# Kernel optimization log

Hardware: AMD Instinct MI355X
Metric: run time of the kernel (lower is better)

Reference implementation:

```python
import jax, jax.numpy as jnp
import numpy as np

BS, IC, L = 8, 64, 32768
OC, K = 64, 3
STRIDE, PAD, DIL = 1, 1, 1
ALPHA = 0.5  # SmoothQuant scaling_factor
QMAX = 127.0  # symmetric int8 fake quant


def fake_quant(t):
    # per-tensor symmetric int8 fake quantization with straight-through estimator
    amax = jnp.max(jnp.abs(jax.lax.stop_gradient(t)))
    s = jnp.where(amax == 0, 1.0, amax / QMAX)
    q = jnp.clip(jnp.round(t / s), -QMAX, QMAX) * s
    return t + jax.lax.stop_gradient(q - t)


def setup_inputs() -> dict:
    key = jax.random.key(0)
    k1, k2, k3 = jax.random.split(key, 3)
    x = jax.random.normal(k1, (BS, IC, L), dtype=jnp.float32)
    weight = jax.random.normal(k2, (OC, IC, K), dtype=jnp.float32) * 0.05
    bias = jax.random.normal(k3, (OC,), dtype=jnp.float32) * 0.01
    return {"x": x, "weight": weight, "bias": bias}


def reference(x, weight, bias):
    bs, ic, length = x.shape
    out_len = (length + 2 * PAD - DIL * (K - 1) - 1) // STRIDE + 1
    # im2col / unfold: (bs, ic, K, out_len) with F.unfold's channel-major, kernel-pos-minor order
    xp = jnp.pad(x, ((0, 0), (0, 0), (PAD, PAD)))
    patches = jnp.stack(
        [xp[:, :, j * DIL : j * DIL + STRIDE * (out_len - 1) + 1 : STRIDE] for j in range(K)],
        axis=2,
    )  # (bs, ic, K, out_len)
    cols = patches.reshape(bs, ic * K, out_len).transpose(0, 2, 1).reshape(bs * out_len, ic * K)
    w = weight.reshape(OC, ic * K)
    # dynamic SmoothQuant scales (detached in original)
    w_scale = jnp.max(jnp.abs(jax.lax.stop_gradient(w)), axis=0)        # (ic*K,)
    act_scale = jnp.max(jnp.abs(jax.lax.stop_gradient(cols)), axis=0)   # (ic*K,)
    scale = act_scale ** ALPHA / w_scale ** (1.0 - ALPHA)
    scale = jnp.where(scale == 0, 1.0, scale)
    xq = fake_quant(cols / scale)
    wq = fake_quant(w * scale)
    out = xq @ wq.T  # (bs*out_len, OC)
    out = out.reshape(bs, out_len, OC).transpose(0, 2, 1) + bias[None, :, None]
    return out
```

## Files before the change

### kernel.cpp

```cpp
#include <hip/hip_runtime.h>

#define L_LEN 32768
#define QMAXF 127.0f
#define TPB 4

typedef __attribute__((ext_vector_type(4))) int v4i;


__global__ __launch_bounds__(1024) void actamax_kernel(const float* __restrict__ x,
                                                       float* __restrict__ wsf) {
    const int ic = blockIdx.x, b = blockIdx.y;
    const float4* row = (const float4*)(x + ((size_t)(b*64 + ic) << 15));
    float mA = 0.0f, mNF = 0.0f, mNL = 0.0f;
    #pragma unroll
    for (int i = 0; i < 8; ++i) {
        int f = threadIdx.x + (i << 10);
        float4 v = row[f];
        float ax = fabsf(v.x), ay = fabsf(v.y), az = fabsf(v.z), aw = fabsf(v.w);
        float m4 = fmaxf(fmaxf(ax, ay), fmaxf(az, aw));
        mA = fmaxf(mA, m4);
        if (f == 0) {
            mNF = fmaxf(mNF, fmaxf(ay, fmaxf(az, aw)));
            mNL = fmaxf(mNL, m4);
        } else if (f == 8191) {
            mNF = fmaxf(mNF, m4);
            mNL = fmaxf(mNL, fmaxf(ax, fmaxf(ay, az)));
        } else {
            mNF = fmaxf(mNF, m4);
            mNL = fmaxf(mNL, m4);
        }
    }
    #pragma unroll
    for (int off = 32; off; off >>= 1) {
        mA  = fmaxf(mA,  __shfl_down(mA,  off));
        mNF = fmaxf(mNF, __shfl_down(mNF, off));
        mNL = fmaxf(mNL, __shfl_down(mNL, off));
    }
    __shared__ float red[3][16];
    int wid = threadIdx.x >> 6;
    if ((threadIdx.x & 63) == 0) { red[0][wid] = mA; red[1][wid] = mNF; red[2][wid] = mNL; }
    __syncthreads();
    if (threadIdx.x == 0) {
        mA = red[0][0]; mNF = red[1][0]; mNL = red[2][0];
        #pragma unroll
        for (int i = 1; i < 16; ++i) {
            mA  = fmaxf(mA,  red[0][i]);
            mNF = fmaxf(mNF, red[1][i]);
            mNL = fmaxf(mNL, red[2][i]);
        }
        float* p = wsf + (ic*8 + b)*3;
        p[0] = mNL; p[1] = mA; p[2] = mNF;
    }
}

__global__ __launch_bounds__(256) void prep_kernel(const float* __restrict__ w,
                                                   float* __restrict__ wsf,
                                                   unsigned int* __restrict__ wsa) {
    __shared__ float scl[192];
    __shared__ float red[256];
    const int tid = threadIdx.x;
    float ax = 0.0f, aw = 0.0f;
    if (tid < 192) {
        float wsc = 0.0f;
        #pragma unroll 8
        for (int o = 0; o < 64; ++o) wsc = fmaxf(wsc, fabsf(w[o*192 + tid]));
        int ic = tid / 3, k = tid - ic*3;
        float asc = 0.0f;
        #pragma unroll
        for (int b = 0; b < 8; ++b) asc = fmaxf(asc, wsf[(ic*8 + b)*3 + k]);
        float sc = sqrtf(asc) / sqrtf(wsc);
        if (sc == 0.0f) sc = 1.0f;
        scl[tid] = sc;
        ax = asc / sc;
        aw = wsc * sc;
    }
    red[tid] = ax; __syncthreads();
    for (int s = 128; s; s >>= 1) { if (tid < s) red[tid] = fmaxf(red[tid], red[tid+s]); __syncthreads(); }
    float axm = red[0]; __syncthreads();
    red[tid] = aw; __syncthreads();
    for (int s = 128; s; s >>= 1) { if (tid < s) red[tid] = fmaxf(red[tid], red[tid+s]); __syncthreads(); }
    float awm = red[0];
    float s_x = (axm == 0.0f) ? 1.0f : axm / QMAXF;
    float s_w = (awm == 0.0f) ? 1.0f : awm / QMAXF;
    if (tid < 192) wsf[1536 + tid] = 1.0f / (scl[tid] * s_x);
    if (tid == 0)  wsf[1728] = s_x * s_w;
    __syncthreads();
    for (int idx = tid; idx < 3072; idx += 256) {
        int oc = idx / 48, dwi = idx - oc*48, j0 = dwi*4;
        unsigned pk = 0;
        #pragma unroll
        for (int bb = 0; bb < 4; ++bb) {
            int j = j0 + bb;
            float q = rintf((w[oc*192 + j] * scl[j]) / s_w);
            q = fminf(fmaxf(q, -QMAXF), QMAXF);
            pk |= (((unsigned)(int)q) & 255u) << (8*bb);
        }
        int mt = oc >> 4, m = oc & 15, c = j0 >> 4, s = c >> 2, kq = c & 3;
        wsa[((mt*3 + s)*64 + kq*16 + m)*4 + ((j0 & 15) >> 2)] = pk;
    }
}

__global__ __launch_bounds__(256) void conv_mfma_kernel(const float* __restrict__ x,
                                                        const float* __restrict__ bias,
                                                        const float* __restrict__ wsf,
                                                        const v4i* __restrict__ wsa,
                                                        float* __restrict__ out) {
    __shared__ int bsm[3072];
    const int tid  = threadIdx.x;
    const int b    = blockIdx.y;
    const int lane = tid & 63;
    const int wv   = tid >> 6;

    const int tq  = tid & 15;
    const int icg = tid >> 4;
    const int tb  = tq << 2;

    float xv[4][6];
    {
        const int t0 = (blockIdx.x * TPB) << 6;
        #pragma unroll
        for (int ici = 0; ici < 4; ++ici) {
            const float* rowp = x + (((size_t)(b*64 + icg*4 + ici)) << 15) + t0 + tb;
            float4 mid = *(const float4*)rowp;
            float lm = (t0 + tb > 0)           ? rowp[-1] : 0.0f;
            float rp = (t0 + tb + 4 < L_LEN)   ? rowp[4]  : 0.0f;
            xv[ici][0] = lm;    xv[ici][1] = mid.x; xv[ici][2] = mid.y;
            xv[ici][3] = mid.z; xv[ici][4] = mid.w; xv[ici][5] = rp;
        }
    }

    v4i afrag[12];
    #pragma unroll
    for (int i = 0; i < 12; ++i) afrag[i] = wsa[i*64 + lane];

    float rv[12];
    #pragma unroll
    for (int jj = 0; jj < 12; ++jj) rv[jj] = wsf[1536 + icg*12 + jj];
    const float sxw = wsf[1728];

    for (int it = 0; it < TPB; ++it) {
        const int t0c = (blockIdx.x * TPB + it) << 6;

        unsigned pkq[12];
        #pragma unroll
        for (int dt = 0; dt < 4; ++dt) {
            #pragma unroll
            for (int dw = 0; dw < 3; ++dw) {
                unsigned pk = 0;
                #pragma unroll
                for (int bb = 0; bb < 4; ++bb) {
                    int jloc = dw*4 + bb;
                    int ici = jloc / 3, k = jloc - ici*3;
                    float q = rintf(xv[ici][dt + k] * rv[jloc]);
                    q = fminf(fmaxf(q, -QMAXF), QMAXF);
                    pk |= (((unsigned)(int)q) & 255u) << (8*bb);
                }
                pkq[dt*3 + dw] = pk;
            }
        }

        if (it) __syncthreads();
        #pragma unroll
        for (int dt = 0; dt < 4; ++dt) {
            int t = tb + dt, wt = t >> 4, n = t & 15;
            #pragma unroll
            for (int dw = 0; dw < 3; ++dw) {
                int j0 = icg*12 + dw*4;
                int c = j0 >> 4, s = c >> 2, kq = c & 3;
                int G = (wt*3 + s)*64 + kq*16 + n;
                G ^= (G >> 6) & 7;
                bsm[G*4 + ((j0 & 15) >> 2)] = (int)pkq[dt*3 + dw];
            }
        }
        __syncthreads();

        if (it + 1 < TPB) {
            const int t0n = (blockIdx.x * TPB + it + 1) << 6;
            #pragma unroll
            for (int ici = 0; ici < 4; ++ici) {
                const float* rowp = x + (((size_t)(b*64 + icg*4 + ici)) << 15) + t0n + tb;
                float4 mid = *(const float4*)rowp;
                float lm = (t0n + tb > 0)          ? rowp[-1] : 0.0f;
                float rp = (t0n + tb + 4 < L_LEN)  ? rowp[4]  : 0.0f;
                xv[ici][0] = lm;    xv[ici][1] = mid.x; xv[ici][2] = mid.y;
                xv[ici][3] = mid.z; xv[ici][4] = mid.w; xv[ici][5] = rp;
            }
        }

        v4i acc[4];
        #pragma unroll
        for (int mt = 0; mt < 4; ++mt) acc[mt] = (v4i){0,0,0,0};
        const v4i* bsmv = (const v4i*)bsm;
        #pragma unroll
        for (int s = 0; s < 3; ++s) {
            int Gr = (wv*3 + s)*64 + lane;
            Gr ^= (wv*3 + s) & 7;
            v4i bf = bsmv[Gr];
            #pragma unroll
            for (int mt = 0; mt < 4; ++mt)
                acc[mt] = __builtin_amdgcn_mfma_i32_16x16x64_i8(afrag[mt*3 + s], bf, acc[mt], 0, 0, 0);
        }

        const int tg   = t0c + (wv << 4) + (lane & 15);
        const int rowq = (lane >> 4) << 2;
        #pragma unroll
        for (int mt = 0; mt < 4; ++mt) {
            #pragma unroll
            for (int i = 0; i < 4; ++i) {
                int oc = mt*16 + rowq + i;
                out[(((size_t)(b*64 + oc)) << 15) + tg] = (float)acc[mt][i] * sxw + bias[oc];
            }
        }
    }
}

extern "C" void kernel_launch(void* const* d_in, const int* in_sizes, int n_in,
                              void* d_out, int out_size, void* d_ws, size_t ws_size,
                              hipStream_t stream) {
    const float* x    = (const float*)d_in[0];
    const float* w    = (const float*)d_in[1];
    const float* bias = (const float*)d_in[2];
    float* out = (float*)d_out;
    float* wsf = (float*)d_ws;
    unsigned int* wsa = (unsigned int*)((char*)d_ws + 8192);

    hipLaunchKernelGGL(actamax_kernel,   dim3(64, 8),       dim3(1024), 0, stream, x, wsf);
    hipLaunchKernelGGL(prep_kernel,      dim3(1),           dim3(256),  0, stream, w, wsf, wsa);
    hipLaunchKernelGGL(conv_mfma_kernel, dim3(512/TPB, 8),  dim3(256),  0, stream,
                       x, bias, wsf, (const v4i*)wsa, out);
}
```

Baseline: 150.5 us.

## Build MFMA B-fragments directly in registers, dropping LDS staging

The weight fragment packing is reordered so each lane's K-dimension groups map channels (16*g+4*d+bb) per kernel tap. The conv kernel can then quantize its activation B-fragment straight from global loads: each lane does unaligned float4 loads over 16 channel rows and packs int8 values in registers. This removes the shared-memory staging, both barriers and the swizzled LDS writes and reads. In exchange it issues more redundant, unaligned global loads, since each element is read by several lanes with overlapping windows, and adds boundary-case branches.

```diff
diff --git a/kernel.cpp b/kernel.cpp
--- a/kernel.cpp
+++ b/kernel.cpp
@@ -2,9 +2,16 @@
 
 #define L_LEN 32768
 #define QMAXF 127.0f
-#define TPB 4
+#define TPW 4
 
 typedef __attribute__((ext_vector_type(4))) int v4i;
+typedef float v4f __attribute__((ext_vector_type(4)));
+
+__device__ inline v4f load4u(const float* p) {
+    v4f v;
+    __builtin_memcpy(&v, p, 16);
+    return v;
+}
 
 
 __global__ __launch_bounds__(1024) void actamax_kernel(const float* __restrict__ x,
@@ -82,21 +89,26 @@
     float awm = red[0];
     float s_x = (axm == 0.0f) ? 1.0f : axm / QMAXF;
     float s_w = (awm == 0.0f) ? 1.0f : awm / QMAXF;
-    if (tid < 192) wsf[1536 + tid] = 1.0f / (scl[tid] * s_x);
+    if (tid < 192) {
+        int k = tid >> 6, ic = tid & 63;
+        wsf[1536 + tid] = 1.0f / (scl[3*ic + k] * s_x);
+    }
     if (tid == 0)  wsf[1728] = s_x * s_w;
     __syncthreads();
     for (int idx = tid; idx < 3072; idx += 256) {
-        int oc = idx / 48, dwi = idx - oc*48, j0 = dwi*4;
+        int d = idx & 3, lane = (idx >> 2) & 63, f = idx >> 8;
+        int mt = f / 3, s = f - mt*3;
+        int g = lane >> 4, m = lane & 15, oc = mt*16 + m;
         unsigned pk = 0;
         #pragma unroll
         for (int bb = 0; bb < 4; ++bb) {
-            int j = j0 + bb;
+            int ic = 16*g + 4*d + bb;
+            int j = 3*ic + s;
             float q = rintf((w[oc*192 + j] * scl[j]) / s_w);
             q = fminf(fmaxf(q, -QMAXF), QMAXF);
             pk |= (((unsigned)(int)q) & 255u) << (8*bb);
         }
-        int mt = oc >> 4, m = oc & 15, c = j0 >> 4, s = c >> 2, kq = c & 3;
-        wsa[((mt*3 + s)*64 + kq*16 + m)*4 + ((j0 & 15) >> 2)] = pk;
+        wsa[idx] = pk;
     }
 }
 
@@ -105,110 +117,93 @@
                                                         const float* __restrict__ wsf,
                                                         const v4i* __restrict__ wsa,
                                                         float* __restrict__ out) {
-    __shared__ int bsm[3072];
     const int tid  = threadIdx.x;
     const int b    = blockIdx.y;
     const int lane = tid & 63;
     const int wv   = tid >> 6;
-
-    const int tq  = tid & 15;
-    const int icg = tid >> 4;
-    const int tb  = tq << 2;
-
-    float xv[4][6];
-    {
-        const int t0 = (blockIdx.x * TPB) << 6;
-        #pragma unroll
-        for (int ici = 0; ici < 4; ++ici) {
-            const float* rowp = x + (((size_t)(b*64 + icg*4 + ici)) << 15) + t0 + tb;
-            float4 mid = *(const float4*)rowp;
-            float lm = (t0 + tb > 0)           ? rowp[-1] : 0.0f;
-            float rp = (t0 + tb + 4 < L_LEN)   ? rowp[4]  : 0.0f;
-            xv[ici][0] = lm;    xv[ici][1] = mid.x; xv[ici][2] = mid.y;
-            xv[ici][3] = mid.z; xv[ici][4] = mid.w; xv[ici][5] = rp;
-        }
-    }
+    const int g    = lane >> 4;
+    const int tl   = lane & 15;
+    const int wgid = blockIdx.x * 4 + wv;
 
     v4i afrag[12];
     #pragma unroll
     for (int i = 0; i < 12; ++i) afrag[i] = wsa[i*64 + lane];
 
-    float rv[12];
-    #pragma unroll
-    for (int jj = 0; jj < 12; ++jj) rv[jj] = wsf[1536 + icg*12 + jj];
+    float rvf[3][16];
+    #pragma unroll
+    for (int s = 0; s < 3; ++s) {
+        #pragma unroll
+        for (int d = 0; d < 4; ++d) {
+            v4f rv4 = *(const v4f*)&wsf[1536 + s*64 + g*16 + d*4];
+            rvf[s][4*d+0] = rv4.x; rvf[s][4*d+1] = rv4.y;
+            rvf[s][4*d+2] = rv4.z; rvf[s][4*d+3] = rv4.w;
+        }
+    }
     const float sxw = wsf[1728];
-
-    for (int it = 0; it < TPB; ++it) {
-        const int t0c = (blockIdx.x * TPB + it) << 6;
-
-        unsigned pkq[12];
-        #pragma unroll
-        for (int dt = 0; dt < 4; ++dt) {
-            #pragma unroll
-            for (int dw = 0; dw < 3; ++dw) {
-                unsigned pk = 0;
+    v4f bsv[4];
+    #pragma unroll
+    for (int mt = 0; mt < 4; ++mt) bsv[mt] = *(const v4f*)&bias[mt*16 + g*4];
+
+    const float* xrow = x + (((size_t)(b*64 + g*16)) << 15);
+
+    for (int it = 0; it < TPW; ++it) {
+        const int tg0 = wgid * (TPW*16) + it*16;
+        const int t   = tg0 + tl;
+
+        unsigned pk[3][4] = {{0,0,0,0},{0,0,0,0},{0,0,0,0}};
+        if (tg0 != 0 && tg0 != L_LEN - 16) {
+            const float* px = xrow + (t - 1);
+            #pragma unroll
+            for (int r = 0; r < 16; ++r) {
+                v4f v = load4u(px + ((size_t)r << 15));
                 #pragma unroll
-                for (int bb = 0; bb < 4; ++bb) {
-                    int jloc = dw*4 + bb;
-                    int ici = jloc / 3, k = jloc - ici*3;
-                    float q = rintf(xv[ici][dt + k] * rv[jloc]);
+                for (int s = 0; s < 3; ++s) {
+                    float xval = (s == 0) ? v.x : (s == 1) ? v.y : v.z;
+                    float q = rintf(xval * rvf[s][r]);
                     q = fminf(fmaxf(q, -QMAXF), QMAXF);
-                    pk |= (((unsigned)(int)q) & 255u) << (8*bb);
+                    pk[s][r >> 2] |= (((unsigned)(int)q) & 255u) << (8*(r & 3));
                 }
-                pkq[dt*3 + dw] = pk;
             }
-        }
-
-        if (it) __syncthreads();
-        #pragma unroll
-        for (int dt = 0; dt < 4; ++dt) {
-            int t = tb + dt, wt = t >> 4, n = t & 15;
-            #pragma unroll
-            for (int dw = 0; dw < 3; ++dw) {
-                int j0 = icg*12 + dw*4;
-                int c = j0 >> 4, s = c >> 2, kq = c & 3;
-                int G = (wt*3 + s)*64 + kq*16 + n;
-                G ^= (G >> 6) & 7;
-                bsm[G*4 + ((j0 & 15) >> 2)] = (int)pkq[dt*3 + dw];
+        } else {
+            const int off = (t == 0) ? 0 : ((t >= L_LEN - 3) ? (L_LEN - 4) : (t - 1));
+            const bool e0  = (t == 0);
+            const bool em2 = (t == L_LEN - 2), em1 = (t == L_LEN - 1);
+            const float* px = xrow + off;
+            #pragma unroll
+            for (int r = 0; r < 16; ++r) {
+                v4f v = load4u(px + ((size_t)r << 15));
+                float x0 = e0 ? 0.0f : (em2 ? v.y : (em1 ? v.z : v.x));
+                float x1 = e0 ? v.x  : (em2 ? v.z : (em1 ? v.w : v.y));
+                float x2 = e0 ? v.y  : (em2 ? v.w : (em1 ? 0.0f : v.z));
+                #pragma unroll
+                for (int s = 0; s < 3; ++s) {
+                    float xval = (s == 0) ? x0 : (s == 1) ? x1 : x2;
+                    float q = rintf(xval * rvf[s][r]);
+                    q = fminf(fmaxf(q, -QMAXF), QMAXF);
+                    pk[s][r >> 2] |= (((unsigned)(int)q) & 255u) << (8*(r & 3));
+                }
             }
         }
-        __syncthreads();
-
-        if (it + 1 < TPB) {
-            const int t0n = (blockIdx.x * TPB + it + 1) << 6;
-            #pragma unroll
-            for (int ici = 0; ici < 4; ++ici) {
-                const float* rowp = x + (((size_t)(b*64 + icg*4 + ici)) << 15) + t0n + tb;
-                float4 mid = *(const float4*)rowp;
-                float lm = (t0n + tb > 0)          ? rowp[-1] : 0.0f;
-                float rp = (t0n + tb + 4 < L_LEN)  ? rowp[4]  : 0.0f;
-                xv[ici][0] = lm;    xv[ici][1] = mid.x; xv[ici][2] = mid.y;
-                xv[ici][3] = mid.z; xv[ici][4] = mid.w; xv[ici][5] = rp;
-            }
-        }
 
         v4i acc[4];
         #pragma unroll
         for (int mt = 0; mt < 4; ++mt) acc[mt] = (v4i){0,0,0,0};
-        const v4i* bsmv = (const v4i*)bsm;
         #pragma unroll
         for (int s = 0; s < 3; ++s) {
-            int Gr = (wv*3 + s)*64 + lane;
-            Gr ^= (wv*3 + s) & 7;
-            v4i bf = bsmv[Gr];
+            v4i bfv;
+            bfv[0] = (int)pk[s][0]; bfv[1] = (int)pk[s][1];
+            bfv[2] = (int)pk[s][2]; bfv[3] = (int)pk[s][3];
             #pragma unroll
             for (int mt = 0; mt < 4; ++mt)
-                acc[mt] = __builtin_amdgcn_mfma_i32_16x16x64_i8(afrag[mt*3 + s], bf, acc[mt], 0, 0, 0);
-        }
-
-        const int tg   = t0c + (wv << 4) + (lane & 15);
-        const int rowq = (lane >> 4) << 2;
+                acc[mt] = __builtin_amdgcn_mfma_i32_16x16x64_i8(afrag[mt*3 + s], bfv, acc[mt], 0, 0, 0);
+        }
+
         #pragma unroll
         for (int mt = 0; mt < 4; ++mt) {
             #pragma unroll
             for (int i = 0; i < 4; ++i) {
-                int oc = mt*16 + rowq + i;
-                out[(((size_t)(b*64 + oc)) << 15) + tg] = (float)acc[mt][i] * sxw + bias[oc];
+                int oc = mt*16 + g*4 + i;
+                out[(((size_t)(b*64 + oc)) << 15) + t] = (float)acc[mt][i] * sxw + bsv[mt][i];
             }
         }
     }
@@ -224,8 +219,8 @@
     float* wsf = (float*)d_ws;
     unsigned int* wsa = (unsigned int*)((char*)d_ws + 8192);
 
-    hipLaunchKernelGGL(actamax_kernel,   dim3(64, 8),       dim3(1024), 0, stream, x, wsf);
-    hipLaunchKernelGGL(prep_kernel,      dim3(1),           dim3(256),  0, stream, w, wsf, wsa);
-    hipLaunchKernelGGL(conv_mfma_kernel, dim3(512/TPB, 8),  dim3(256),  0, stream,
+    hipLaunchKernelGGL(actamax_kernel,   dim3(64, 8),  dim3(1024), 0, stream, x, wsf);
+    hipLaunchKernelGGL(prep_kernel,      dim3(1),      dim3(256),  0, stream, w, wsf, wsa);
+    hipLaunchKernelGGL(conv_mfma_kernel, dim3(128, 8), dim3(256),  0, stream,
                        x, bias, wsf, (const v4i*)wsa, out);
 }
```

New measurement: 174.8 us. +16.2%, slower.

## Fuse scale prep into amax kernel via last-block atomic, double-buffer LDS

Applied to the files above, without the earlier changes.

Merges the single-block prep kernel into the activation amax kernel. The last block to finish, detected with an atomic counter, computes the SmoothQuant scales and quantized weights using 1024 threads and shuffle reductions. This removes one kernel launch and the serial single-block tail. The conv kernel now double-buffers its LDS tile, which drops one barrier per iteration. The change adds a memset launch and relies on threadfence/atomic ordering for correctness.

```diff
diff --git a/kernel.cpp b/kernel.cpp
--- a/kernel.cpp
+++ b/kernel.cpp
@@ -7,14 +7,18 @@
 typedef __attribute__((ext_vector_type(4))) int v4i;
 
 
-__global__ __launch_bounds__(1024) void actamax_kernel(const float* __restrict__ x,
-                                                       float* __restrict__ wsf) {
+__global__ __launch_bounds__(1024) void actamax_prep_kernel(const float* __restrict__ x,
+                                                            const float* __restrict__ w,
+                                                            float* __restrict__ wsf,
+                                                            unsigned int* __restrict__ wsa,
+                                                            unsigned int* __restrict__ cnt) {
     const int ic = blockIdx.x, b = blockIdx.y;
+    const int tid = threadIdx.x;
     const float4* row = (const float4*)(x + ((size_t)(b*64 + ic) << 15));
     float mA = 0.0f, mNF = 0.0f, mNL = 0.0f;
     #pragma unroll
     for (int i = 0; i < 8; ++i) {
-        int f = threadIdx.x + (i << 10);
+        int f = tid + (i << 10);
         float4 v = row[f];
         float ax = fabsf(v.x), ay = fabsf(v.y), az = fabsf(v.z), aw = fabsf(v.w);
         float m4 = fmaxf(fmaxf(ax, ay), fmaxf(az, aw));
@@ -37,10 +41,11 @@
         mNL = fmaxf(mNL, __shfl_down(mNL, off));
     }
     __shared__ float red[3][16];
-    int wid = threadIdx.x >> 6;
-    if ((threadIdx.x & 63) == 0) { red[0][wid] = mA; red[1][wid] = mNF; red[2][wid] = mNL; }
-    __syncthreads();
-    if (threadIdx.x == 0) {
+    __shared__ int lastf;
+    int wid = tid >> 6;
+    if ((tid & 63) == 0) { red[0][wid] = mA; red[1][wid] = mNF; red[2][wid] = mNL; }
+    __syncthreads();
+    if (tid == 0) {
         mA = red[0][0]; mNF = red[1][0]; mNL = red[2][0];
         #pragma unroll
         for (int i = 1; i < 16; ++i) {
@@ -50,42 +55,58 @@
         }
         float* p = wsf + (ic*8 + b)*3;
         p[0] = mNL; p[1] = mA; p[2] = mNF;
-    }
-}
-
-__global__ __launch_bounds__(256) void prep_kernel(const float* __restrict__ w,
-                                                   float* __restrict__ wsf,
-                                                   unsigned int* __restrict__ wsa) {
+        __threadfence();
+        unsigned int t = __hip_atomic_fetch_add(cnt, 1u, __ATOMIC_ACQ_REL,
+                                                __HIP_MEMORY_SCOPE_AGENT);
+        lastf = (t == 511);
+    }
+    __syncthreads();
+    if (!lastf) return;
+
+    __threadfence();
     __shared__ float scl[192];
-    __shared__ float red[256];
-    const int tid = threadIdx.x;
+    __shared__ float redA[16], redW[16];
+    __shared__ float bc[2];
     float ax = 0.0f, aw = 0.0f;
-    if (tid < 192) {
+    if (tid < 768) {
+        int col = tid >> 2, sub = tid & 3;
         float wsc = 0.0f;
-        #pragma unroll 8
-        for (int o = 0; o < 64; ++o) wsc = fmaxf(wsc, fabsf(w[o*192 + tid]));
-        int ic = tid / 3, k = tid - ic*3;
-        float asc = 0.0f;
-        #pragma unroll
-        for (int b = 0; b < 8; ++b) asc = fmaxf(asc, wsf[(ic*8 + b)*3 + k]);
-        float sc = sqrtf(asc) / sqrtf(wsc);
-        if (sc == 0.0f) sc = 1.0f;
-        scl[tid] = sc;
-        ax = asc / sc;
-        aw = wsc * sc;
-    }
-    red[tid] = ax; __syncthreads();
-    for (int s = 128; s; s >>= 1) { if (tid < s) red[tid] = fmaxf(red[tid], red[tid+s]); __syncthreads(); }
-    float axm = red[0]; __syncthreads();
-    red[tid] = aw; __syncthreads();
-    for (int s = 128; s; s >>= 1) { if (tid < s) red[tid] = fmaxf(red[tid], red[tid+s]); __syncthreads(); }
-    float awm = red[0];
-    float s_x = (axm == 0.0f) ? 1.0f : axm / QMAXF;
-    float s_w = (awm == 0.0f) ? 1.0f : awm / QMAXF;
+        #pragma unroll
+        for (int o = 0; o < 16; ++o) wsc = fmaxf(wsc, fabsf(w[(sub*16 + o)*192 + col]));
+        wsc = fmaxf(wsc, __shfl_xor(wsc, 1));
+        wsc = fmaxf(wsc, __shfl_xor(wsc, 2));
+        if (sub == 0) {
+            int ici = col / 3, k = col - ici*3;
+            float asc = 0.0f;
+            #pragma unroll
+            for (int bb = 0; bb < 8; ++bb) asc = fmaxf(asc, wsf[(ici*8 + bb)*3 + k]);
+            float sc = sqrtf(asc) / sqrtf(wsc);
+            if (sc == 0.0f) sc = 1.0f;
+            scl[col] = sc;
+            ax = asc / sc;
+            aw = wsc * sc;
+        }
+    }
+    #pragma unroll
+    for (int off = 32; off; off >>= 1) {
+        ax = fmaxf(ax, __shfl_down(ax, off));
+        aw = fmaxf(aw, __shfl_down(aw, off));
+    }
+    if ((tid & 63) == 0) { redA[wid] = ax; redW[wid] = aw; }
+    __syncthreads();
+    if (tid == 0) {
+        float axm = redA[0], awm = redW[0];
+        #pragma unroll
+        for (int i = 1; i < 16; ++i) { axm = fmaxf(axm, redA[i]); awm = fmaxf(awm, redW[i]); }
+        bc[0] = axm; bc[1] = awm;
+    }
+    __syncthreads();
+    const float s_x = (bc[0] == 0.0f) ? 1.0f : bc[0] / QMAXF;
+    const float s_w = (bc[1] == 0.0f) ? 1.0f : bc[1] / QMAXF;
     if (tid < 192) wsf[1536 + tid] = 1.0f / (scl[tid] * s_x);
     if (tid == 0)  wsf[1728] = s_x * s_w;
     __syncthreads();
-    for (int idx = tid; idx < 3072; idx += 256) {
+    for (int idx = tid; idx < 3072; idx += 1024) {
         int oc = idx / 48, dwi = idx - oc*48, j0 = dwi*4;
         unsigned pk = 0;
         #pragma unroll
@@ -105,7 +126,7 @@
                                                         const float* __restrict__ wsf,
                                                         const v4i* __restrict__ wsa,
                                                         float* __restrict__ out) {
-    __shared__ int bsm[3072];
+    __shared__ int bsm[2][3072];
     const int tid  = threadIdx.x;
     const int b    = blockIdx.y;
     const int lane = tid & 63;
@@ -140,6 +161,7 @@
 
     for (int it = 0; it < TPB; ++it) {
         const int t0c = (blockIdx.x * TPB + it) << 6;
+        const int buf = it & 1;
 
         unsigned pkq[12];
         #pragma unroll
@@ -159,7 +181,6 @@
             }
         }
 
-        if (it) __syncthreads();
         #pragma unroll
         for (int dt = 0; dt < 4; ++dt) {
             int t = tb + dt, wt = t >> 4, n = t & 15;
@@ -169,7 +190,7 @@
                 int c = j0 >> 4, s = c >> 2, kq = c & 3;
                 int G = (wt*3 + s)*64 + kq*16 + n;
                 G ^= (G >> 6) & 7;
-                bsm[G*4 + ((j0 & 15) >> 2)] = (int)pkq[dt*3 + dw];
+                bsm[buf][G*4 + ((j0 & 15) >> 2)] = (int)pkq[dt*3 + dw];
             }
         }
         __syncthreads();
@@ -190,7 +211,7 @@
         v4i acc[4];
         #pragma unroll
         for (int mt = 0; mt < 4; ++mt) acc[mt] = (v4i){0,0,0,0};
-        const v4i* bsmv = (const v4i*)bsm;
+        const v4i* bsmv = (const v4i*)bsm[buf];
         #pragma unroll
         for (int s = 0; s < 3; ++s) {
             int Gr = (wv*3 + s)*64 + lane;
@@ -223,9 +244,11 @@
     float* out = (float*)d_out;
     float* wsf = (float*)d_ws;
     unsigned int* wsa = (unsigned int*)((char*)d_ws + 8192);
-
-    hipLaunchKernelGGL(actamax_kernel,   dim3(64, 8),       dim3(1024), 0, stream, x, wsf);
-    hipLaunchKernelGGL(prep_kernel,      dim3(1),           dim3(256),  0, stream, w, wsf, wsa);
-    hipLaunchKernelGGL(conv_mfma_kernel, dim3(512/TPB, 8),  dim3(256),  0, stream,
+    unsigned int* cnt = (unsigned int*)((char*)d_ws + 7168);
+
+    hipMemsetAsync(cnt, 0, 4, stream);
+    hipLaunchKernelGGL(actamax_prep_kernel, dim3(64, 8),  dim3(1024), 0, stream,
+                       x, w, wsf, wsa, cnt);
+    hipLaunchKernelGGL(conv_mfma_kernel,    dim3(128, 8), dim3(256),  0, stream,
                        x, bias, wsf, (const v4i*)wsa, out);
 }
```

After: 171.2 us. 13.8% more time.

## Split activation amax across chunks with atomics and double-buffer conv LDS

Applied to the files above, without the earlier changes.

The activation amax kernel now splits each row into 4 chunks over a third grid dimension, using 256-thread blocks that issue all 8 float4 loads before reducing. Partial maxima are combined with atomicMax on the float bits, with a memset beforehand to zero the workspace. The conv kernel double-buffers its shared B tile, which removes the barrier before each tile write. The cost is an extra memset call, atomics, and twice the LDS per conv block.

```diff
diff --git a/kernel.cpp b/kernel.cpp
--- a/kernel.cpp
+++ b/kernel.cpp
@@ -7,15 +7,26 @@
 typedef __attribute__((ext_vector_type(4))) int v4i;
 
 
-__global__ __launch_bounds__(1024) void actamax_kernel(const float* __restrict__ x,
-                                                       float* __restrict__ wsf) {
-    const int ic = blockIdx.x, b = blockIdx.y;
+__device__ inline void amax_atomic(float* p, float v) {
+    atomicMax((unsigned int*)p, __float_as_uint(v));
+}
+
+__global__ __launch_bounds__(256) void actamax_kernel(const float* __restrict__ x,
+                                                      float* __restrict__ wsf) {
+    const int ic = blockIdx.x, b = blockIdx.y, ch = blockIdx.z;
+    const int tid = threadIdx.x;
     const float4* row = (const float4*)(x + ((size_t)(b*64 + ic) << 15));
+    const int base = ch*2048 + tid;
+
+    float4 vbuf[8];
+    #pragma unroll
+    for (int i = 0; i < 8; ++i) vbuf[i] = row[base + i*256];
+
     float mA = 0.0f, mNF = 0.0f, mNL = 0.0f;
     #pragma unroll
     for (int i = 0; i < 8; ++i) {
-        int f = threadIdx.x + (i << 10);
-        float4 v = row[f];
+        const int f = base + i*256;
+        float4 v = vbuf[i];
         float ax = fabsf(v.x), ay = fabsf(v.y), az = fabsf(v.z), aw = fabsf(v.w);
         float m4 = fmaxf(fmaxf(ax, ay), fmaxf(az, aw));
         mA = fmaxf(mA, m4);
@@ -36,20 +47,18 @@
         mNF = fmaxf(mNF, __shfl_down(mNF, off));
         mNL = fmaxf(mNL, __shfl_down(mNL, off));
     }
-    __shared__ float red[3][16];
-    int wid = threadIdx.x >> 6;
-    if ((threadIdx.x & 63) == 0) { red[0][wid] = mA; red[1][wid] = mNF; red[2][wid] = mNL; }
+    __shared__ float red[3][4];
+    const int wid = tid >> 6;
+    if ((tid & 63) == 0) { red[0][wid] = mA; red[1][wid] = mNF; red[2][wid] = mNL; }
     __syncthreads();
-    if (threadIdx.x == 0) {
-        mA = red[0][0]; mNF = red[1][0]; mNL = red[2][0];
-        #pragma unroll
-        for (int i = 1; i < 16; ++i) {
-            mA  = fmaxf(mA,  red[0][i]);
-            mNF = fmaxf(mNF, red[1][i]);
-            mNL = fmaxf(mNL, red[2][i]);
-        }
+    if (tid == 0) {
+        mA  = fmaxf(fmaxf(red[0][0], red[0][1]), fmaxf(red[0][2], red[0][3]));
+        mNF = fmaxf(fmaxf(red[1][0], red[1][1]), fmaxf(red[1][2], red[1][3]));
+        mNL = fmaxf(fmaxf(red[2][0], red[2][1]), fmaxf(red[2][2], red[2][3]));
         float* p = wsf + (ic*8 + b)*3;
-        p[0] = mNL; p[1] = mA; p[2] = mNF;
+        amax_atomic(p + 0, mNL);
+        amax_atomic(p + 1, mA);
+        amax_atomic(p + 2, mNF);
     }
 }
 
@@ -105,7 +114,7 @@
                                                         const float* __restrict__ wsf,
                                                         const v4i* __restrict__ wsa,
                                                         float* __restrict__ out) {
-    __shared__ int bsm[3072];
+    __shared__ int bsm[2][3072];
     const int tid  = threadIdx.x;
     const int b    = blockIdx.y;
     const int lane = tid & 63;
@@ -140,6 +149,7 @@
 
     for (int it = 0; it < TPB; ++it) {
         const int t0c = (blockIdx.x * TPB + it) << 6;
+        const int buf = it & 1;
 
         unsigned pkq[12];
         #pragma unroll
@@ -159,7 +169,6 @@
             }
         }
 
-        if (it) __syncthreads();
         #pragma unroll
         for (int dt = 0; dt < 4; ++dt) {
             int t = tb + dt, wt = t >> 4, n = t & 15;
@@ -169,7 +178,7 @@
                 int c = j0 >> 4, s = c >> 2, kq = c & 3;
                 int G = (wt*3 + s)*64 + kq*16 + n;
                 G ^= (G >> 6) & 7;
-                bsm[G*4 + ((j0 & 15) >> 2)] = (int)pkq[dt*3 + dw];
+                bsm[buf][G*4 + ((j0 & 15) >> 2)] = (int)pkq[dt*3 + dw];
             }
         }
         __syncthreads();
@@ -190,7 +199,7 @@
         v4i acc[4];
         #pragma unroll
         for (int mt = 0; mt < 4; ++mt) acc[mt] = (v4i){0,0,0,0};
-        const v4i* bsmv = (const v4i*)bsm;
+        const v4i* bsmv = (const v4i*)bsm[buf];
         #pragma unroll
         for (int s = 0; s < 3; ++s) {
             int Gr = (wv*3 + s)*64 + lane;
@@ -224,8 +233,9 @@
     float* wsf = (float*)d_ws;
     unsigned int* wsa = (unsigned int*)((char*)d_ws + 8192);
 
-    hipLaunchKernelGGL(actamax_kernel,   dim3(64, 8),       dim3(1024), 0, stream, x, wsf);
-    hipLaunchKernelGGL(prep_kernel,      dim3(1),           dim3(256),  0, stream, w, wsf, wsa);
-    hipLaunchKernelGGL(conv_mfma_kernel, dim3(512/TPB, 8),  dim3(256),  0, stream,
+    hipMemsetAsync(wsf, 0, 6144, stream);
+    hipLaunchKernelGGL(actamax_kernel,   dim3(64, 8, 4), dim3(256), 0, stream, x, wsf);
+    hipLaunchKernelGGL(prep_kernel,      dim3(1),        dim3(256), 0, stream, w, wsf, wsa);
+    hipLaunchKernelGGL(conv_mfma_kernel, dim3(128, 8),   dim3(256), 0, stream,
                        x, bias, wsf, (const v4i*)wsa, out);
 }
```

After: 152.1 us. No clear change (+1.1%).
